# Kernel optimization log

Measured on AMD Instinct MI355X. Metric: run time of the kernel, lower is better.

The kernel has to match this reference:

```python
import jax, jax.numpy as jnp
import numpy as np
import math

TOPK = 13
NC = 80
ALPHA = 1.0
BETA = 6.0
EPS = 1e-9


def _xyxy2wh(b):
    return b[..., 2:4] - b[..., 0:2]


def _bbox_ciou(box1, box2, eps=1e-7):
    # box1: [bs,nmax,1,4] gt, box2: [bs,1,na,4] pred, xyxy. Returns [bs,nmax,na].
    b1x1, b1y1, b1x2, b1y2 = jnp.split(box1, 4, axis=-1)
    b2x1, b2y1, b2x2, b2y2 = jnp.split(box2, 4, axis=-1)
    w1, h1 = b1x2 - b1x1, b1y2 - b1y1 + eps
    w2, h2 = b2x2 - b2x1, b2y2 - b2y1 + eps
    inter = jnp.clip(jnp.minimum(b1x2, b2x2) - jnp.maximum(b1x1, b2x1), 0) * \
            jnp.clip(jnp.minimum(b1y2, b2y2) - jnp.maximum(b1y1, b2y1), 0)
    union = w1 * h1 + w2 * h2 - inter + eps
    iou = inter / union
    cw = jnp.maximum(b1x2, b2x2) - jnp.minimum(b1x1, b2x1)  # enclosing box
    ch = jnp.maximum(b1y2, b2y2) - jnp.minimum(b1y1, b2y1)
    c2 = cw ** 2 + ch ** 2 + eps
    rho2 = ((b2x1 + b2x2 - b1x1 - b1x2) ** 2 + (b2y1 + b2y2 - b1y1 - b1y2) ** 2) / 4.0
    v = (4.0 / math.pi ** 2) * (jnp.arctan(w2 / h2) - jnp.arctan(w1 / h1)) ** 2
    a = jax.lax.stop_gradient(v / (v - iou + (1.0 + eps)))  # torch.no_grad alpha
    return (iou - (rho2 / c2 + v * a))[..., 0]


def tal_forward(pd_scores, pd_bboxes, anc_points, gt_labels, gt_bboxes, mask_gt,
                gt_kkpts, pd_kkpts, sigma, stride_tensor, reg_max):
    bs, na, nc = pd_scores.shape
    nmax = gt_bboxes.shape[1]
    dt = pd_scores.dtype
    mgt = mask_gt[..., 0]  # [bs,nmax]

    # --- select_candidates_in_gts: anchor center strictly inside gt box ---
    lt = gt_bboxes[:, :, None, :2]              # [bs,nmax,1,2]
    rb = gt_bboxes[:, :, None, 2:]
    anc = anc_points[None, None]                # [1,1,na,2]
    deltas = jnp.concatenate([anc - lt, rb - anc], -1)  # [bs,nmax,na,4]
    mask_in_gts = (deltas.min(-1) > EPS).astype(dt)

    # --- my_filter_anchor: anchor max predictable box edge >= gt mean edge ---
    aps_max = stride_tensor[:, 0] * (reg_max - 1) * 2          # [na]
    gt_size = _xyxy2wh(gt_bboxes).mean(-1)                     # [bs,nmax] (w+h)/2
    filt = (aps_max[None, None, :] - gt_size[..., None] >= EPS).astype(dt)
    mask_in_gts = mask_in_gts * filt

    m = mask_in_gts * mask_gt  # [bs,nmax,na] float 0/1 (mask_in_gts * mask_gt)

    # --- get_box_metrics ---
    lbl = gt_labels[..., 0].astype(jnp.int32)                  # [bs,nmax]
    onehot = jax.nn.one_hot(lbl, nc, dtype=dt)
    bbox_scores = jnp.einsum('bnc,bgc->bgn', pd_scores, onehot) * m

    iou = jnp.clip(_bbox_ciou(gt_bboxes[:, :, None, :], pd_bboxes[:, None, :, :]), 0)

    # OKS-style keypoint iou (my_kpt_iou)
    area = (_xyxy2wh(gt_bboxes).prod(-1) * 0.53)[:, :, None, None]   # [bs,nmax,1,1]
    kmask = (gt_kkpts[..., 2] != 0)[:, :, None, :].astype(dt)        # [bs,nmax,1,nk]
    d = (pd_kkpts[:, None, :, :, 0] - gt_kkpts[:, :, None, :, 0]) ** 2 + \
        (pd_kkpts[:, None, :, :, 1] - gt_kkpts[:, :, None, :, 1]) ** 2  # [bs,nmax,na,nk]
    e = d / ((2.0 * sigma) ** 2) / (area + 1e-7) / 2.0
    kpt_iou = (jnp.exp(-e) * kmask).sum(-1) / (kmask.sum(-1) + 1e-7)
    kpt_iou = jnp.clip(kpt_iou, 0)

    overlaps = ((iou + kpt_iou) / 2.0) * m
    align_metric = (bbox_scores ** ALPHA) * (overlaps ** BETA)

    # --- select_topk_candidates ---
    topk_mask = jnp.broadcast_to(mgt[:, :, None] > 0, (bs, nmax, TOPK))
    _, idxs = jax.lax.top_k(align_metric, TOPK)                # [bs,nmax,TOPK]
    idxs = jnp.where(topk_mask, idxs, 0)
    flat = idxs.reshape(bs * nmax, TOPK)
    cnt = jnp.zeros((bs * nmax, na), jnp.int32).at[
        jnp.arange(bs * nmax)[:, None], flat].add(1)
    cnt = cnt.reshape(bs, nmax, na)
    mask_topk = jnp.where(cnt > 1, 0, cnt).astype(dt)          # drop duplicated idx 0

    mask_pos = mask_topk * mask_in_gts * mask_gt

    # --- select_highest_overlaps ---
    fg = mask_pos.sum(-2)                                      # [bs,na]
    multi = fg[:, None, :] > 1
    is_max = jax.nn.one_hot(overlaps.argmax(1), nmax, dtype=dt).transpose(0, 2, 1)
    mask_pos = jnp.where(multi, is_max, mask_pos)
    fg = mask_pos.sum(-2)
    tgi = mask_pos.argmax(-2)                                  # [bs,na] target gt idx

    # --- get_targets ---
    flat_idx = tgi + jnp.arange(bs, dtype=tgi.dtype)[:, None] * nmax
    tlabels = jnp.clip(gt_labels.reshape(-1)[flat_idx], 0)     # [bs,na]
    tbboxes = gt_bboxes.reshape(-1, 4)[flat_idx]               # [bs,na,4]
    tscores = jax.nn.one_hot(tlabels, nc, dtype=dt)
    tscores = jnp.where(fg[..., None] > 0, tscores, 0.0)

    # --- normalize scores by aligned metric ---
    align_metric = align_metric * mask_pos
    pos_align = align_metric.max(-1, keepdims=True)            # [bs,nmax,1]
    pos_ov = (overlaps * mask_pos).max(-1, keepdims=True)
    norm = (align_metric * pos_ov / (pos_align + EPS)).max(-2)[..., None]  # [bs,na,1]
    tscores = tscores * norm
    return tlabels, tbboxes, tscores, fg > 0, tgi


def setup_inputs() -> dict:
    key = jax.random.key(0)
    ks = jax.random.split(key, 10)
    bs, nmax, nc, nk = 16, 64, 80, 1
    pts, strs = [], []
    for s, n in [(8, 80), (16, 40), (32, 20)]:
        g = (jnp.arange(n, dtype=jnp.float32) + 0.5) * s
        yv, xv = jnp.meshgrid(g, g, indexing='ij')
        pts.append(jnp.stack([xv.ravel(), yv.ravel()], -1))
        strs.append(jnp.full((n * n, 1), float(s), jnp.float32))
    anc_points = jnp.concatenate(pts, 0)        # [8400,2]
    stride_tensor = jnp.concatenate(strs, 0)    # [8400,1]
    na = anc_points.shape[0]

    def boxes(k, shape):
        k1, k2 = jax.random.split(k)
        c = jax.random.uniform(k1, shape + (2,), jnp.float32, 60.0, 580.0)
        wh = jax.random.uniform(k2, shape + (2,), jnp.float32, 10.0, 120.0)
        return jnp.concatenate([c - wh / 2, c + wh / 2], -1)

    pd_scores = jax.random.uniform(ks[0], (bs, na, nc), jnp.float32)
    pd_bboxes = boxes(ks[1], (bs, na))
    gt_bboxes = boxes(ks[2], (bs, nmax))
    gt_labels = jax.random.randint(ks[3], (bs, nmax, 1), 0, nc)
    mask_gt = (jax.random.uniform(ks[4], (bs, nmax, 1)) < 0.7).astype(jnp.float32)
    gt_xy = jax.random.uniform(ks[5], (bs, nmax, nk, 2), jnp.float32, 0.0, 640.0)
    gt_v = jax.random.randint(ks[6], (bs, nmax, nk, 1), 0, 3).astype(jnp.float32)
    gt_kkpts = jnp.concatenate([gt_xy, gt_v], -1)
    pd_xy = jax.random.uniform(ks[7], (bs, na, nk, 2), jnp.float32, 0.0, 640.0)
    pd_v = jax.random.uniform(ks[8], (bs, na, nk, 1), jnp.float32)
    pd_kkpts = jnp.concatenate([pd_xy, pd_v], -1)
    sigma = jnp.full((nk,), 0.25, jnp.float32)
    return dict(pd_scores=pd_scores, pd_bboxes=pd_bboxes, anc_points=anc_points,
                gt_labels=gt_labels, gt_bboxes=gt_bboxes, mask_gt=mask_gt,
                gt_kkpts=gt_kkpts, pd_kkpts=pd_kkpts, sigma=sigma,
                stride_tensor=stride_tensor, reg_max=16)


def reference(pd_scores, pd_bboxes, anc_points, gt_labels, gt_bboxes, mask_gt,
              gt_kkpts, pd_kkpts, sigma, stride_tensor, reg_max):
    return tal_forward(pd_scores, pd_bboxes, anc_points, gt_labels, gt_bboxes,
                       mask_gt, gt_kkpts, pd_kkpts, sigma, stride_tensor, reg_max)
```

## Files before the change

kernel.cpp:

```cpp
#include <hip/hip_runtime.h>
#include <math.h>
#include <float.h>
#include <limits.h>

#define TOPK 13
typedef unsigned int u32;
typedef unsigned long long u64;

__device__ __forceinline__ u32 q32f(double x) {
  if (!(x > 0.0)) return 0u;
  float f = (float)x;
  u32 b = __float_as_uint(f);
  return (b >= 0x00800000u) ? b : 0u;
}
__device__ __forceinline__ double val32(u32 b) {
  return (double)__uint_as_float(b);
}

struct MetricQ { u32 amb; u32 ovb; bool m; };

__device__ MetricQ metric_at(
    const float* __restrict__ pd_scores, const float* __restrict__ pd_bboxes,
    const float* __restrict__ anc, const int* __restrict__ gt_labels,
    const float* __restrict__ gt_bboxes, const float* __restrict__ mask_gt,
    const float* __restrict__ gt_kkpts, const float* __restrict__ pd_kkpts,
    const float* __restrict__ sigma, const float* __restrict__ stride_t,
    int reg_max, int b, int g, int a, int nmax, int na, int nc, int nk)
{
#pragma clang fp contract(off)
  MetricQ r; r.amb = 0u; r.ovb = 0u; r.m = false;
  const float* gb = gt_bboxes + (size_t)(b * nmax + g) * 4;
  float gx1 = gb[0], gy1 = gb[1], gx2 = gb[2], gy2 = gb[3];
  float mgt = mask_gt[b * nmax + g];
  float ax = anc[(size_t)a * 2 + 0], ay = anc[(size_t)a * 2 + 1];
  float dmin = fminf(fminf(ax - gx1, ay - gy1), fminf(gx2 - ax, gy2 - ay));
  float aps = (stride_t[a] * (float)(reg_max - 1)) * 2.0f;
  float gw = gx2 - gx1, gh = gy2 - gy1;
  float gsize = (gw + gh) * 0.5f;
  bool mm = ((double)dmin > 1e-9) && ((double)(aps - gsize) >= 1e-9) && (mgt > 0.f);
  r.m = mm;
  if (!mm) return r;

  int lbl = gt_labels[b * nmax + g];
  float score = pd_scores[((size_t)(b * na + a)) * nc + lbl];

  const float* pb = pd_bboxes + ((size_t)(b * na + a)) * 4;
  float px1 = pb[0], py1 = pb[1], px2 = pb[2], py2 = pb[3];
  const float e7 = 1e-7f;
  float w1 = gx2 - gx1, h1 = (gy2 - gy1) + e7;
  float w2 = px2 - px1, h2 = (py2 - py1) + e7;
  float iw = fmaxf(fminf(gx2, px2) - fmaxf(gx1, px1), 0.f);
  float ih = fmaxf(fminf(gy2, py2) - fmaxf(gy1, py1), 0.f);
  float inter = iw * ih;
  float uni = ((w1 * h1 + w2 * h2) - inter) + e7;
  float iou = inter / uni;
  float cw = fmaxf(gx2, px2) - fminf(gx1, px1);
  float ch = fmaxf(gy2, py2) - fminf(gy1, py1);
  float c2 = (cw * cw + ch * ch) + e7;
  float dcx = ((px1 + px2) - gx1) - gx2;
  float dcy = ((py1 + py2) - gy1) - gy2;
  float rho2 = (dcx * dcx + dcy * dcy) / 4.0f;
  float a2 = (float)atan((double)(w2 / h2));
  float a1 = (float)atan((double)(w1 / h1));
  float arc = a2 - a1;
  const float C = (float)(4.0 / (3.14159265358979323846 * 3.14159265358979323846));
  float v = C * (arc * arc);
  const float C1 = (float)(1.0 + 1e-7);
  float al = v / ((v - iou) + C1);
  float ciou = iou - (rho2 / c2 + v * al);
  float iouc = fmaxf(ciou, 0.f);

  float area = (gw * gh) * 0.53f;
  double ksum = 0.0;
  float  kcnt = 0.f;
  for (int k = 0; k < nk; k++) {
    const float* gk = gt_kkpts + ((size_t)(b * nmax + g) * nk + k) * 3;
    const float* pk = pd_kkpts + (((size_t)(b * na + a)) * nk + k) * 3;
    float km = (gk[2] != 0.f) ? 1.f : 0.f;
    float dx = pk[0] - gk[0], dy = pk[1] - gk[1];
    float d  = dx * dx + dy * dy;
    float s2 = 2.f * sigma[k]; s2 = s2 * s2;
    float e1 = d / s2;
    float e2 = e1 / (area + 1e-7f);
    float e  = e2 / 2.0f;
    double s1 = val32(q32f(exp(-(double)e)));
    double term = s1 * (double)km;
    ksum = val32(q32f(ksum + term));
    kcnt = kcnt + km;
  }
  double den = (double)(kcnt + 1e-7f);
  u32 kioub = q32f(ksum / den);
  double kiou = val32(kioub);
  u32 sumb = q32f((double)iouc + kiou);
  u32 ovlb = q32f(val32(sumb) * 0.5);
  double ovl = val32(ovlb);
  u32 p6b = q32f(pow(ovl, 6.0));
  u32 amb = q32f((double)score * val32(p6b));
  r.ovb = ovlb;
  r.amb = amb;
  return r;
}

__global__ void k_zero4(float* __restrict__ p, long n4) {
  long i = (long)blockIdx.x * blockDim.x + threadIdx.x;
  if (i < n4) ((float4*)p)[i] = make_float4(0.f, 0.f, 0.f, 0.f);
}
__global__ void k_zeroi(int* __restrict__ p, long n) {
  long i = (long)blockIdx.x * blockDim.x + threadIdx.x;
  if (i < n) p[i] = 0;
}

#define MAXC 512

__global__ void k_rows(const float* __restrict__ pd_scores, const float* __restrict__ pd_bboxes,
                       const float* __restrict__ anc, const int* __restrict__ gt_labels,
                       const float* __restrict__ gt_bboxes, const float* __restrict__ mask_gt,
                       const float* __restrict__ gt_kkpts, const float* __restrict__ pd_kkpts,
                       const float* __restrict__ sigma, const float* __restrict__ stride_t,
                       const int* __restrict__ reg_max_p,
                       int* __restrict__ cnt, int* __restrict__ gsel,
                       u32* __restrict__ amsel, u32* __restrict__ ovsel,
                       int bs, int nmax, int na, int nc, int nk)
{
  int g = blockIdx.x, b = blockIdx.y;
  if (mask_gt[b * nmax + g] <= 0.f) return;
  int reg_max = reg_max_p[0];
  int tid = threadIdx.x;
  int wave = tid >> 6, lane = tid & 63;

  __shared__ int   s_ncand;
  __shared__ int   s_cand[MAXC];
  __shared__ u32   s_keyv[MAXC];
  __shared__ u32   s_ovv[MAXC];
  __shared__ unsigned short s_ciOf[1024];
  __shared__ u32   s_bitPos[32];
  __shared__ u64   s_red[4];
  __shared__ u64   s_win;
  __shared__ int   s_selA[TOPK];
  __shared__ int   s_selCi[TOPK];

  if (tid == 0) s_ncand = 0;
  if (tid < 32) s_bitPos[tid] = 0u;
  for (int i = tid; i < 1024; i += 256) s_ciOf[i] = 0xFFFF;
  __syncthreads();

  {
    const float* gb = gt_bboxes + (size_t)(b * nmax + g) * 4;
    float gx1 = gb[0], gy1 = gb[1], gx2 = gb[2], gy2 = gb[3];
    float gw = gx2 - gx1, gh = gy2 - gy1;
    float gsize = (gw + gh) * 0.5f;
    for (int a = tid; a < na; a += 256) {
      float ax = anc[(size_t)a * 2 + 0], ay = anc[(size_t)a * 2 + 1];
      float dmin = fminf(fminf(ax - gx1, ay - gy1), fminf(gx2 - ax, gy2 - ay));
      float aps = (stride_t[a] * (float)(reg_max - 1)) * 2.0f;
      bool mm = ((double)dmin > 1e-9) && ((double)(aps - gsize) >= 1e-9);
      if (mm) {
        int ci = atomicAdd(&s_ncand, 1);
        if (ci < MAXC) {
          s_cand[ci] = a;
          if (a < 1024) s_ciOf[a] = (unsigned short)ci;
        }
      }
    }
  }
  __syncthreads();
  int ncand = min(s_ncand, MAXC);

  for (int ci = tid; ci < ncand; ci += 256) {
    int a = s_cand[ci];
    MetricQ mt = metric_at(pd_scores, pd_bboxes, anc, gt_labels, gt_bboxes, mask_gt,
                           gt_kkpts, pd_kkpts, sigma, stride_t, reg_max,
                           b, g, a, nmax, na, nc, nk);
    s_keyv[ci] = mt.amb;
    s_ovv[ci]  = mt.ovb;
    if (mt.amb != 0u && a < 1024) atomicOr(&s_bitPos[a >> 5], 1u << (a & 31));
  }
  __syncthreads();

  u32 pk = 0xFFFFFFFFu; int pi = -1;
  int npos = TOPK;
  for (int k = 0; k < TOPK; k++) {
    u32 bK = 0u; int bA = INT_MAX; int bCi = -1;
    for (int ci = tid; ci < ncand; ci += 256) {
      u32 vv = s_keyv[ci]; int a = s_cand[ci];
      if (vv < pk || (vv == pk && a > pi)) {
        if (vv > bK || (vv == bK && a < bA)) { bK = vv; bA = a; bCi = ci; }
      }
    }
    u64 p = ((u64)bK << 32) | (u64)(u32)(0xFFFFFFFFu - (u32)bA);
    for (int off = 32; off; off >>= 1) {
      u64 q = __shfl_xor(p, off);
      if (q > p) p = q;
    }
    if (lane == 0) s_red[wave] = p;
    __syncthreads();
    if (tid == 0) {
      u64 w = s_red[0];
      for (int i = 1; i < 4; i++) if (s_red[i] > w) w = s_red[i];
      s_win = w;
    }
    __syncthreads();
    u64 win = s_win;
    u32 wK = (u32)(win >> 32);
    if (wK == 0u) { npos = k; break; }
    int wA = (int)(0xFFFFFFFFu - (u32)(win & 0xFFFFFFFFu));
    if (p == win && bCi >= 0 && bK == wK && bA == wA) {
      s_selCi[k] = bCi; s_selA[k] = wA;
    }
    pk = wK; pi = wA;
    __syncthreads();
  }

  __syncthreads();
  if (tid == 0) {
    int a = 0;
    for (int k = npos; k < TOPK; k++) {
      while ((s_bitPos[a >> 5] >> (a & 31)) & 1u) a++;
      s_selA[k] = a;
      s_selCi[k] = (s_ciOf[a] == 0xFFFF) ? -1 : (int)s_ciOf[a];
      a++;
    }
  }
  __syncthreads();

  if (tid < TOPK) {
    int ci = s_selCi[tid];
    if (ci >= 0) {
      int a = s_selA[tid];
      int t = b * na + a;
      atomicAdd(&cnt[t], 1);
      gsel[t] = g;
      amsel[t] = s_keyv[ci];
      ovsel[t] = s_ovv[ci];
    }
  }
}

__global__ void k_anchors(const int* __restrict__ gt_labels, const float* __restrict__ gt_bboxes,
                          const int* __restrict__ cnt, const int* __restrict__ gsel,
                          const u32* __restrict__ amsel, const u32* __restrict__ ovsel,
                          u32* __restrict__ pa, u32* __restrict__ po,
                          u32* __restrict__ amfin, float* __restrict__ out,
                          int* __restrict__ mcount, int* __restrict__ mlist,
                          int bs, int nmax, int na, int nc,
                          long tb_off, long fg_off, long tgi_off)
{
  int t = blockIdx.x * blockDim.x + threadIdx.x;
  if (t >= bs * na) return;
  int b = t / na;

  int c = cnt[t];
  if (c > 1) {
    int i = atomicAdd(mcount, 1);
    mlist[i] = t;
    return;
  }
  int tgi = 0; u32 amb = 0u, ovb = 0u; bool fg = false;
  if (c == 1) { tgi = gsel[t]; amb = amsel[t]; ovb = ovsel[t]; fg = true; }

  int lbl = gt_labels[b * nmax + tgi]; if (lbl < 0) lbl = 0;
  out[t] = (float)lbl;
  const float* gb = gt_bboxes + (size_t)(b * nmax + tgi) * 4;
  float* tb = out + tb_off + (long)t * 4;
  tb[0] = gb[0]; tb[1] = gb[1]; tb[2] = gb[2]; tb[3] = gb[3];
  out[fg_off + t] = fg ? 1.0f : 0.0f;
  out[tgi_off + t] = (float)tgi;

  amfin[t] = amb;
  if (fg) {
    int row = b * nmax + tgi;
    atomicMax(&pa[row], amb);
    atomicMax(&po[row], ovb);
  }
}

__global__ void k_multi(const float* __restrict__ pd_scores, const float* __restrict__ pd_bboxes,
                        const float* __restrict__ anc, const int* __restrict__ gt_labels,
                        const float* __restrict__ gt_bboxes, const float* __restrict__ mask_gt,
                        const float* __restrict__ gt_kkpts, const float* __restrict__ pd_kkpts,
                        const float* __restrict__ sigma, const float* __restrict__ stride_t,
                        const int* __restrict__ reg_max_p,
                        const int* __restrict__ mcount, const int* __restrict__ mlist,
                        u32* __restrict__ pa, u32* __restrict__ po,
                        u32* __restrict__ amfin, float* __restrict__ out,
                        int bs, int nmax, int na, int nc, int nk,
                        long tb_off, long fg_off, long tgi_off)
{
  int waveId = (int)((blockIdx.x * blockDim.x + threadIdx.x) >> 6);
  int lane   = threadIdx.x & 63;
  int nwaves = (int)((gridDim.x * blockDim.x) >> 6);
  int reg_max = reg_max_p[0];
  int M = mcount[0];

  for (int i = waveId; i < M; i += nwaves) {
    int t = mlist[i];
    int b = t / na, a = t - b * na;
    u32 ovg = 0u, amg = 0u;
    if (lane < nmax) {
      MetricQ mt = metric_at(pd_scores, pd_bboxes, anc, gt_labels, gt_bboxes, mask_gt,
                             gt_kkpts, pd_kkpts, sigma, stride_t, reg_max,
                             b, lane, a, nmax, na, nc, nk);
      ovg = mt.m ? mt.ovb : 0u;
      amg = mt.m ? mt.amb : 0u;
    }
    u64 p = ((u64)ovg << 32) | (u64)(u32)(0xFFFFFFFFu - (u32)lane);
    for (int off = 32; off; off >>= 1) {
      u64 q = __shfl_xor(p, off);
      if (q > p) p = q;
    }
    int wg = (int)(0xFFFFFFFFu - (u32)(p & 0xFFFFFFFFu));
    if (lane == wg) {
      int lbl = gt_labels[b * nmax + wg]; if (lbl < 0) lbl = 0;
      out[t] = (float)lbl;
      const float* gb = gt_bboxes + (size_t)(b * nmax + wg) * 4;
      float* tb = out + tb_off + (long)t * 4;
      tb[0] = gb[0]; tb[1] = gb[1]; tb[2] = gb[2]; tb[3] = gb[3];
      out[fg_off + t] = 1.0f;
      out[tgi_off + t] = (float)wg;
      amfin[t] = amg;
      int row = b * nmax + wg;
      atomicMax(&pa[row], amg);
      atomicMax(&po[row], ovg);
    }
  }
}

__global__ void k_scores(const u32* __restrict__ pa, const u32* __restrict__ po,
                         const u32* __restrict__ amfin, float* __restrict__ out,
                         int bs, int nmax, int na, int nc, long ts_off, long fg_off, long tgi_off)
{
  int t = blockIdx.x * blockDim.x + threadIdx.x;
  if (t >= bs * na) return;
  if (out[fg_off + t] <= 0.f) return;
  int b = t / na;
  int tgi = (int)out[tgi_off + t];
  int row = b * nmax + tgi;
  u32 rb = q32f(val32(po[row]) / (val32(pa[row]) + (double)1e-9f));
  u32 nb = q32f(val32(amfin[t]) * val32(rb));
  int lbl = (int)out[t];
  out[ts_off + (long)t * nc + lbl] = __uint_as_float(nb);
}

extern "C" void kernel_launch(void* const* d_in, const int* in_sizes, int n_in,
                              void* d_out, int out_size, void* d_ws, size_t ws_size,
                              hipStream_t stream) {
  const float* pd_scores = (const float*)d_in[0];
  const float* pd_bboxes = (const float*)d_in[1];
  const float* anc       = (const float*)d_in[2];
  const int*   gt_labels = (const int*)  d_in[3];
  const float* gt_bboxes = (const float*)d_in[4];
  const float* mask_gt   = (const float*)d_in[5];
  const float* gt_kkpts  = (const float*)d_in[6];
  const float* pd_kkpts  = (const float*)d_in[7];
  const float* sigma     = (const float*)d_in[8];
  const float* stride_t  = (const float*)d_in[9];
  const int*   reg_max_p = (const int*)  d_in[10];

  int na   = in_sizes[2] / 2;
  int bs   = in_sizes[1] / (na * 4);
  int nc   = in_sizes[0] / (bs * na);
  int nmax = in_sizes[3] / bs;
  int nk   = in_sizes[8];

  long nba = (long)bs * na;
  int  R   = bs * nmax;

  int* cnt    = (int*)d_ws;
  u32* pa     = (u32*)(cnt + nba);
  u32* po     = pa + R;
  int* mcount = (int*)(po + R);
  int* gsel   = mcount + 64;
  u32* amsel  = (u32*)(gsel + nba);
  u32* ovsel  = amsel + nba;
  u32* amfin  = ovsel + nba;
  int* mlist  = (int*)(amfin + nba);

  float* out = (float*)d_out;
  long tb_off  = nba;
  long ts_off  = nba * 5;
  long fg_off  = ts_off + nba * nc;
  long tgi_off = fg_off + nba;

  long nz = nba + 2L * R + 64;
  k_zeroi<<<(int)((nz + 255) / 256), 256, 0, stream>>>(cnt, nz);
  long n4 = (nba * nc) / 4;
  k_zero4<<<(int)((n4 + 255) / 256), 256, 0, stream>>>(out + ts_off, n4);

  dim3 grows(nmax, bs);
  k_rows<<<grows, 256, 0, stream>>>(pd_scores, pd_bboxes, anc, gt_labels, gt_bboxes,
                                    mask_gt, gt_kkpts, pd_kkpts, sigma, stride_t,
                                    reg_max_p, cnt, gsel, amsel, ovsel,
                                    bs, nmax, na, nc, nk);

  int nthr = (int)((nba + 255) / 256);
  k_anchors<<<nthr, 256, 0, stream>>>(gt_labels, gt_bboxes, cnt, gsel, amsel, ovsel,
                                      pa, po, amfin, out, mcount, mlist,
                                      bs, nmax, na, nc, tb_off, fg_off, tgi_off);

  k_multi<<<256, 256, 0, stream>>>(pd_scores, pd_bboxes, anc, gt_labels, gt_bboxes,
                                   mask_gt, gt_kkpts, pd_kkpts, sigma, stride_t,
                                   reg_max_p, mcount, mlist, pa, po, amfin, out,
                                   bs, nmax, na, nc, nk, tb_off, fg_off, tgi_off);

  k_scores<<<nthr, 256, 0, stream>>>(pa, po, amfin, out, bs, nmax, na, nc,
                                     ts_off, fg_off, tgi_off);
}
```

Before: 158.0 us.

## Fuse score zeroing into final fill kernel and run top-k selection on one wave

Removes the separate zero-fill kernel for the target score tensor. The final kernel now writes every float4 of the score row, putting the normalized value at the label position and zeros elsewhere, so the large output is written once instead of zeroed and then scattered into. The top-k loop in the per-GT kernel now runs on a single wavefront using only shuffle reductions, which drops the block-wide barriers in each iteration but leaves three waves idle during selection. The normalization order also changes to multiply before divide, which may alter rounding slightly.

```diff
diff --git a/kernel.cpp b/kernel.cpp
--- a/kernel.cpp
+++ b/kernel.cpp
@@ -101,10 +101,6 @@
   return r;
 }
 
-__global__ void k_zero4(float* __restrict__ p, long n4) {
-  long i = (long)blockIdx.x * blockDim.x + threadIdx.x;
-  if (i < n4) ((float4*)p)[i] = make_float4(0.f, 0.f, 0.f, 0.f);
-}
 __global__ void k_zeroi(int* __restrict__ p, long n) {
   long i = (long)blockIdx.x * blockDim.x + threadIdx.x;
   if (i < n) p[i] = 0;
@@ -134,8 +130,6 @@
   __shared__ u32   s_ovv[MAXC];
   __shared__ unsigned short s_ciOf[1024];
   __shared__ u32   s_bitPos[32];
-  __shared__ u64   s_red[4];
-  __shared__ u64   s_win;
   __shared__ int   s_selA[TOPK];
   __shared__ int   s_selCi[TOPK];
 
@@ -177,42 +171,34 @@
   }
   __syncthreads();
 
+  if (wave != 0) return;
+
   u32 pk = 0xFFFFFFFFu; int pi = -1;
   int npos = TOPK;
   for (int k = 0; k < TOPK; k++) {
     u32 bK = 0u; int bA = INT_MAX; int bCi = -1;
-    for (int ci = tid; ci < ncand; ci += 256) {
+    for (int ci = lane; ci < ncand; ci += 64) {
       u32 vv = s_keyv[ci]; int a = s_cand[ci];
       if (vv < pk || (vv == pk && a > pi)) {
         if (vv > bK || (vv == bK && a < bA)) { bK = vv; bA = a; bCi = ci; }
       }
     }
     u64 p = ((u64)bK << 32) | (u64)(u32)(0xFFFFFFFFu - (u32)bA);
+    u64 w = p;
     for (int off = 32; off; off >>= 1) {
-      u64 q = __shfl_xor(p, off);
-      if (q > p) p = q;
-    }
-    if (lane == 0) s_red[wave] = p;
-    __syncthreads();
-    if (tid == 0) {
-      u64 w = s_red[0];
-      for (int i = 1; i < 4; i++) if (s_red[i] > w) w = s_red[i];
-      s_win = w;
-    }
-    __syncthreads();
-    u64 win = s_win;
-    u32 wK = (u32)(win >> 32);
+      u64 q = __shfl_xor(w, off);
+      if (q > w) w = q;
+    }
+    u32 wK = (u32)(w >> 32);
     if (wK == 0u) { npos = k; break; }
-    int wA = (int)(0xFFFFFFFFu - (u32)(win & 0xFFFFFFFFu));
-    if (p == win && bCi >= 0 && bK == wK && bA == wA) {
+    int wA = (int)(0xFFFFFFFFu - (u32)(w & 0xFFFFFFFFu));
+    if (p == w && bCi >= 0 && bK == wK && bA == wA) {
       s_selCi[k] = bCi; s_selA[k] = wA;
     }
     pk = wK; pi = wA;
-    __syncthreads();
-  }
-
-  __syncthreads();
-  if (tid == 0) {
+  }
+
+  if (lane == 0) {
     int a = 0;
     for (int k = npos; k < TOPK; k++) {
       while ((s_bitPos[a >> 5] >> (a & 31)) & 1u) a++;
@@ -221,12 +207,11 @@
       a++;
     }
   }
-  __syncthreads();
-
-  if (tid < TOPK) {
-    int ci = s_selCi[tid];
+
+  if (lane < TOPK) {
+    int ci = s_selCi[lane];
     if (ci >= 0) {
-      int a = s_selA[tid];
+      int a = s_selA[lane];
       int t = b * na + a;
       atomicAdd(&cnt[t], 1);
       gsel[t] = g;
@@ -325,20 +310,32 @@
   }
 }
 
-__global__ void k_scores(const u32* __restrict__ pa, const u32* __restrict__ po,
-                         const u32* __restrict__ amfin, float* __restrict__ out,
-                         int bs, int nmax, int na, int nc, long ts_off, long fg_off, long tgi_off)
+__global__ void k_fill(const u32* __restrict__ pa, const u32* __restrict__ po,
+                       const u32* __restrict__ amfin, float* __restrict__ out,
+                       int bs, int nmax, int na, int nc4,
+                       long ts_off, long fg_off, long tgi_off)
 {
-  int t = blockIdx.x * blockDim.x + threadIdx.x;
-  if (t >= bs * na) return;
-  if (out[fg_off + t] <= 0.f) return;
-  int b = t / na;
-  int tgi = (int)out[tgi_off + t];
-  int row = b * nmax + tgi;
-  u32 rb = q32f(val32(po[row]) / (val32(pa[row]) + (double)1e-9f));
-  u32 nb = q32f(val32(amfin[t]) * val32(rb));
-  int lbl = (int)out[t];
-  out[ts_off + (long)t * nc + lbl] = __uint_as_float(nb);
+  long idx = (long)blockIdx.x * blockDim.x + threadIdx.x;
+  long total = (long)bs * na * nc4;
+  if (idx >= total) return;
+  int q = (int)(idx % nc4);
+  long t = idx / nc4;
+  float4 vv = make_float4(0.f, 0.f, 0.f, 0.f);
+  if (out[fg_off + t] > 0.f) {
+    int lbl = (int)out[t];
+    if ((lbl >> 2) == q) {
+      int b = (int)(t / na);
+      int tgi = (int)out[tgi_off + t];
+      int row = b * nmax + tgi;
+      u32 xb = q32f(val32(amfin[t]) * val32(po[row]));
+      u32 nb = q32f(val32(xb) / (val32(pa[row]) + (double)1e-9f));
+      float nrm = __uint_as_float(nb);
+      int r = lbl & 3;
+      if (r == 0) vv.x = nrm; else if (r == 1) vv.y = nrm;
+      else if (r == 2) vv.z = nrm; else vv.w = nrm;
+    }
+  }
+  ((float4*)(out + ts_off))[idx] = vv;
 }
 
 extern "C" void kernel_launch(void* const* d_in, const int* in_sizes, int n_in,
@@ -383,8 +380,6 @@
 
   long nz = nba + 2L * R + 64;
   k_zeroi<<<(int)((nz + 255) / 256), 256, 0, stream>>>(cnt, nz);
-  long n4 = (nba * nc) / 4;
-  k_zero4<<<(int)((n4 + 255) / 256), 256, 0, stream>>>(out + ts_off, n4);
 
   dim3 grows(nmax, bs);
   k_rows<<<grows, 256, 0, stream>>>(pd_scores, pd_bboxes, anc, gt_labels, gt_bboxes,
@@ -402,6 +397,9 @@
                                    reg_max_p, mcount, mlist, pa, po, amfin, out,
                                    bs, nmax, na, nc, nk, tb_off, fg_off, tgi_off);
 
-  k_scores<<<nthr, 256, 0, stream>>>(pa, po, amfin, out, bs, nmax, na, nc,
-                                     ts_off, fg_off, tgi_off);
-}
+  int nc4 = nc / 4;
+  long totalF4 = nba * nc4;
+  k_fill<<<(int)((totalF4 + 255) / 256), 256, 0, stream>>>(pa, po, amfin, out,
+                                                           bs, nmax, na, nc4,
+                                                           ts_off, fg_off, tgi_off);
+}
```

New measurement: 158.2 us. No clear change (+0.1%).
